# Performance work log

Measured on AMD Instinct MI355X. Metric: run time of the kernel, lower is better.

Reference implementation:

```python
import jax, jax.numpy as jnp
import numpy as np

S = 100        # sos_token_num
H = 12         # num heads
LY = 3         # number of residual blocks
NEG = -100.0   # attention-bias masking value


def layer_norm(x, w, b, eps=1e-5):
    u = jnp.mean(x, -1, keepdims=True)
    v = jnp.mean((x - u) ** 2, -1, keepdims=True)
    return (x - u) / jnp.sqrt(v + eps) * w + b


def quick_gelu(x):
    return x * jax.nn.sigmoid(1.702 * x)


def l2norm(x, eps=1e-12):
    return x / jnp.maximum(jnp.linalg.norm(x, axis=-1, keepdims=True), eps)


def setup_inputs() -> dict:
    key = jax.random.key(0)
    ks = iter(jax.random.split(key, 32))
    n, c, hh, ww, out_dim = 2, 768, 32, 32, 512
    r = lambda shape, s=1.0: jax.random.normal(next(ks), shape, jnp.float32) * s
    return dict(
        cls_token=r((1, n, c)),
        pix_feat=r((n, c, hh, ww)),
        last_surgery=r((1 + hh * ww, n, c)),
        attn_bias=r((n, 1, S, hh, ww)),
        qkv_w=r((LY, 3 * c, c), 0.02), qkv_b=jnp.zeros((LY, 3 * c)),
        proj_w=r((LY, c, c), 0.02), proj_b=jnp.zeros((LY, c)),
        ln1_w=jnp.ones((LY, c)), ln1_b=jnp.zeros((LY, c)),
        ln2_w=jnp.ones((LY, c)), ln2_b=jnp.zeros((LY, c)),
        fc_w=r((LY, 4 * c, c), 0.02), fc_b=jnp.zeros((LY, 4 * c)),
        fc2_w=r((LY, c, 4 * c), 0.02), fc2_b=jnp.zeros((LY, c)),
        lnp_w=jnp.ones((c,)), lnp_b=jnp.zeros((c,)),
        proj_out=r((c, out_dim), 0.02),
    )


def reference(cls_token, pix_feat, last_surgery, attn_bias,
              qkv_w, qkv_b, proj_w, proj_b,
              ln1_w, ln1_b, ln2_w, ln2_b,
              fc_w, fc_b, fc2_w, fc2_b,
              lnp_w, lnp_b, proj_out):
    n, c, hh, ww = pix_feat.shape
    L = hh * ww
    N = S + 1 + L
    d = c // H
    scale = d ** -0.5

    # ---- assemble token streams (batch-first [n, N, c]) ----
    pix_tok = pix_feat.reshape(n, c, L).transpose(2, 0, 1)          # [L, n, c]
    x = jnp.concatenate([jnp.broadcast_to(cls_token, (S, n, c)), cls_token, pix_tok], 0)
    x_sur = jnp.concatenate([jnp.broadcast_to(last_surgery[0:1], (S, n, c)), last_surgery], 0)
    xo = x.transpose(1, 0, 2)      # 'original' stream  [n, N, c]
    xs = x_sur.transpose(1, 0, 2)  # 'surgery'  stream  [n, N, c]

    # ---- build attention biases (identity downsample: bias already at (h, w)) ----
    base = jnp.zeros((N, N), jnp.float32)
    base = base.at[:, :S].set(NEG)
    base = base.at[jnp.arange(S), jnp.arange(S)].set(0.0)
    base = base.at[:S, S].set(NEG)
    plain = jnp.broadcast_to(base, (n, H, N, N))
    bias = jnp.broadcast_to(attn_bias, (n, H, S, hh, ww)).reshape(n, H, S, L)
    biased = plain.at[:, :, :S, S + 1:].set(bias)   # sos rows attend to pixels via bias

    def attention(t, l):
        # t: [n, N, c] (post-ln_1); returns (surgery_res, ori_res)
        qkv = (t @ qkv_w[l].T + qkv_b[l]).reshape(n, N, 3, H, d).transpose(2, 0, 3, 1, 4)
        q, k, v = qkv[0], qkv[1], qkv[2]   # each [n, H, N, d]
        def attend(q_, k_, mask):
            a = jax.nn.softmax(jnp.einsum('bhnd,bhmd->bhnm', q_, k_) * scale + mask, axis=-1)
            o = jnp.einsum('bhnm,bhmd->bhnd', a, v).transpose(0, 2, 1, 3).reshape(n, N, c)
            return o @ proj_w[l].T + proj_b[l]
        x_ori_res = attend(q, k, biased)   # standard pass, biased mask (attn_mask[0])
        x_res = attend(v, v, plain)        # q = k = v surgery pass (attn_mask[1])
        return x_res, x_ori_res

    for l in range(LY):
        t = layer_norm(xo, ln1_w[l], ln1_b[l])
        res_sur, res_ori = attention(t, l)
        xo = xo + res_ori
        xo = xo + (quick_gelu(layer_norm(xo, ln2_w[l], ln2_b[l]) @ fc_w[l].T + fc_b[l]) @ fc2_w[l].T + fc2_b[l])
        xs = xs + res_sur

    # ---- heads ----
    sos = l2norm(layer_norm(xo[:, :S], lnp_w, lnp_b) @ proj_out)          # [n, S, out]
    img = l2norm(layer_norm(xs[:, S:], lnp_w, lnp_b) @ proj_out)          # [n, 1+L, out]
    img = img[:, 1:, :].transpose(0, 2, 1).reshape(n, proj_out.shape[1], hh, ww)
    return sos, img
```

## Files before the change

### kernel.cpp

```cpp
#include <hip/hip_runtime.h>
#include <math.h>


constexpr int Cc = 768;
constexpr int Ss = 100;
constexpr int Hh = 12;
constexpr int Ll = 1024;
constexpr int Nn = 1125;
constexpr int NB = 2;
constexpr float QS = 0.18033688011112042f;
constexpr float LOG2E = 1.4426950408889634f;

typedef unsigned short u16;
typedef __attribute__((ext_vector_type(8))) short short8v;
typedef __attribute__((ext_vector_type(8))) unsigned short ushort8v;
typedef __attribute__((ext_vector_type(4))) float f32x4;
typedef __attribute__((ext_vector_type(4))) unsigned int u32x4;

__device__ inline u16 f2bf(float f) {
  unsigned u = __builtin_bit_cast(unsigned int, f);
  unsigned r = u + 0x7fffu + ((u >> 16) & 1u);
  return (u16)(r >> 16);
}
__device__ inline float bf2f(u16 v) {
  return __builtin_bit_cast(float, (unsigned int)v << 16);
}
__device__ inline unsigned cvtpk(float lo, float hi) {
  unsigned r;
  asm("v_cvt_pk_bf16_f32 %0, %1, %2" : "=v"(r) : "v"(lo), "v"(hi));
  return r;
}

__device__ inline int swz(int row, int col) {
  return (row << 6) + ((((col >> 3) ^ (row & 7)) << 3) | (col & 7));
}

__global__ __launch_bounds__(256) void assemble_kernel(
    const float* __restrict__ cls, const float* __restrict__ pix,
    const float* __restrict__ sur, float* __restrict__ xo, float* __restrict__ xs) {
  int idx = blockIdx.x * 256 + (int)threadIdx.x;
  int total = NB * Nn * Cc;
  if (idx >= total) return;
  int ch = idx % Cc;
  int t  = (idx / Cc) % Nn;
  int b  = idx / (Cc * Nn);
  float vo, vs;
  if (t <= Ss) vo = cls[b * Cc + ch];
  else         vo = pix[(size_t)b * Cc * Ll + (size_t)ch * Ll + (t - Ss - 1)];
  if (t < Ss)  vs = sur[b * Cc + ch];
  else         vs = sur[(size_t)(t - Ss) * NB * Cc + b * Cc + ch];
  xo[idx] = vo;
  xs[idx] = vs;
}

constexpr int CN0 = 3 * 2304 * 768;
constexpr int CN1 = 3 * 768 * 768;
constexpr int CN2 = 3 * 3072 * 768;
constexpr int CN3 = 3 * 768 * 3072;
__global__ __launch_bounds__(256) void cvt4_kernel(
    const float* __restrict__ s0, const float* __restrict__ s1,
    const float* __restrict__ s2, const float* __restrict__ s3,
    u16* __restrict__ dst) {
  int i4 = (blockIdx.x * 256 + (int)threadIdx.x) * 4;
  if (i4 >= CN0 + CN1 + CN2 + CN3) return;
  const float* src; int off;
  if (i4 < CN0)             { src = s0; off = i4; }
  else if (i4 < CN0 + CN1)  { src = s1; off = i4 - CN0; }
  else if (i4 < CN0 + CN1 + CN2) { src = s2; off = i4 - CN0 - CN1; }
  else                      { src = s3; off = i4 - CN0 - CN1 - CN2; }
  float4 v = *(const float4*)(src + off);
  *(ushort4*)(dst + i4) = make_ushort4(f2bf(v.x), f2bf(v.y), f2bf(v.z), f2bf(v.w));
}

__global__ __launch_bounds__(256) void transpose_po_kernel(
    const float* __restrict__ in, u16* __restrict__ out) {
  int id = blockIdx.x * 256 + (int)threadIdx.x;
  if (id >= 512 * 768) return;
  int nidx = id / 768, k = id - nidx * 768;
  out[id] = f2bf(in[(size_t)k * 512 + nidx]);
}

__global__ __launch_bounds__(256) void ln_kernel(
    const float* __restrict__ X, const float* __restrict__ w, const float* __restrict__ b,
    u16* __restrict__ Y, int rows_per_b, int row_off) {
  int r = blockIdx.x;
  int bb = r / rows_per_b;
  int i  = r % rows_per_b;
  const float* x = X + ((size_t)bb * Nn + row_off + i) * Cc;
  u16* y = Y + (size_t)r * Cc;
  int tid = (int)threadIdx.x;
  float v0 = x[tid], v1 = x[tid + 256], v2 = x[tid + 512];
  float s = v0 + v1 + v2;
  __shared__ float sbuf[4];
  for (int off = 32; off; off >>= 1) s += __shfl_xor(s, off);
  if ((tid & 63) == 0) sbuf[tid >> 6] = s;
  __syncthreads();
  float mean = (sbuf[0] + sbuf[1] + sbuf[2] + sbuf[3]) * (1.0f / Cc);
  float d0 = v0 - mean, d1 = v1 - mean, d2 = v2 - mean;
  float q = d0 * d0 + d1 * d1 + d2 * d2;
  __syncthreads();
  for (int off = 32; off; off >>= 1) q += __shfl_xor(q, off);
  if ((tid & 63) == 0) sbuf[tid >> 6] = q;
  __syncthreads();
  float var = (sbuf[0] + sbuf[1] + sbuf[2] + sbuf[3]) * (1.0f / Cc);
  float inv = rsqrtf(var + 1e-5f);
  y[tid]       = f2bf(d0 * inv * w[tid]       + b[tid]);
  y[tid + 256] = f2bf(d1 * inv * w[tid + 256] + b[tid + 256]);
  y[tid + 512] = f2bf(d2 * inv * w[tid + 512] + b[tid + 512]);
}

__global__ __launch_bounds__(256) void gemm64_kernel(
    const u16* __restrict__ A0, const u16* __restrict__ A1,
    const u16* __restrict__ B, const float* __restrict__ bias,
    const float* __restrict__ res0, const float* __restrict__ res1,
    float* __restrict__ outf0, float* __restrict__ outf1,
    u16* __restrict__ outb0, u16* __restrict__ outb1,
    int M, int N, int K, int act) {
  __shared__ __align__(16) u16 Als[64 * 64];
  __shared__ __align__(16) u16 Bls[128 * 64];
  int zz = blockIdx.z;
  const u16* A = zz ? A1 : A0;
  const float* res = zz ? res1 : res0;
  float* outf = zz ? outf1 : outf0;
  u16* outb = zz ? outb1 : outb0;
  int tid = (int)threadIdx.x;
  int wave = tid >> 6, lane = tid & 63, g = lane >> 4, li = lane & 15;
  int row0 = blockIdx.y * 64, col0 = blockIdx.x * 128;

  const u16* aptr[2]; int dA[2];
#pragma unroll
  for (int j = 0; j < 2; ++j) {
    int ca = tid + j * 256;
    int r = ca >> 3, c8 = ca & 7;
    dA[j] = (r << 6) + ((c8 ^ (r & 7)) << 3);
    int ra = row0 + r; if (ra > M - 1) ra = M - 1;
    aptr[j] = A + (size_t)ra * K + (c8 << 3);
  }
  const u16* bptr[4]; int dB[4];
#pragma unroll
  for (int j = 0; j < 4; ++j) {
    int cb = tid + j * 256;
    int r = cb >> 3, c8 = cb & 7;
    dB[j] = (r << 6) + ((c8 ^ (r & 7)) << 3);
    bptr[j] = B + (size_t)(col0 + r) * K + (c8 << 3);
  }

  f32x4 acc[4][2];
#pragma unroll
  for (int mi = 0; mi < 4; ++mi)
#pragma unroll
    for (int ni = 0; ni < 2; ++ni) acc[mi][ni] = (f32x4){0.f, 0.f, 0.f, 0.f};

  for (int k0 = 0; k0 < K; k0 += 64) {
    ushort8v ta[2], tb[4];
#pragma unroll
    for (int j = 0; j < 2; ++j) ta[j] = *(const ushort8v*)(aptr[j] + k0);
#pragma unroll
    for (int j = 0; j < 4; ++j) tb[j] = *(const ushort8v*)(bptr[j] + k0);
    __syncthreads();
#pragma unroll
    for (int j = 0; j < 2; ++j) *(ushort8v*)&Als[dA[j]] = ta[j];
#pragma unroll
    for (int j = 0; j < 4; ++j) *(ushort8v*)&Bls[dB[j]] = tb[j];
    __syncthreads();
#pragma unroll
    for (int kc = 0; kc < 2; ++kc) {
      short8v af[4], bfr[2];
#pragma unroll
      for (int mi = 0; mi < 4; ++mi) {
        int rr = mi * 16 + li;
        af[mi] = *(const short8v*)&Als[(rr << 6) + (((kc * 4 + g) ^ (rr & 7)) << 3)];
      }
#pragma unroll
      for (int ni = 0; ni < 2; ++ni) {
        int rb = wave * 32 + ni * 16 + li;
        bfr[ni] = *(const short8v*)&Bls[(rb << 6) + (((kc * 4 + g) ^ (rb & 7)) << 3)];
      }
#pragma unroll
      for (int mi = 0; mi < 4; ++mi)
#pragma unroll
        for (int ni = 0; ni < 2; ++ni)
          acc[mi][ni] = __builtin_amdgcn_mfma_f32_16x16x32_bf16(af[mi], bfr[ni], acc[mi][ni], 0, 0, 0);
    }
  }

#pragma unroll
  for (int mi = 0; mi < 4; ++mi) {
#pragma unroll
    for (int r = 0; r < 4; ++r) {
      int m = row0 + mi * 16 + g * 4 + r;
      if (m >= M) continue;
#pragma unroll
      for (int ni = 0; ni < 2; ++ni) {
        int n = col0 + wave * 32 + ni * 16 + li;
        float v = acc[mi][ni][r];
        if (bias) v += bias[n];
        if (act)  v = v / (1.0f + __expf(-1.702f * v));
        if (res)  v += res[(size_t)m * N + n];
        if (outf) outf[(size_t)m * N + n] = v;
        else      outb[(size_t)m * N + n] = f2bf(v);
      }
    }
  }
}

__global__ __launch_bounds__(256) void attn_kernel(
    const u16* __restrict__ qkv, const float* __restrict__ abias,
    u16* __restrict__ ao, u16* __restrict__ as_) {
  __shared__ __align__(16) u16 Klds[64 * 64];
  __shared__ __align__(16) u16 Vt[64 * 64];
  int id = (int)blockIdx.x;
  int virt = (id & 7) * 114 + (id >> 3);
  int gid = virt / 19;
  int qt  = virt - gid * 19;
  int z   = gid / 24;
  int bh  = gid - z * 24;
  int b = bh / Hh, h = bh - b * Hh;
  int tid = (int)threadIdx.x;
  int wave = tid >> 6, lane = tid & 63, g = lane >> 4, li = lane & 15;
  bool sosq = qt >= 17;
  u16* outp = z ? as_ : ao;

  int qbase = sosq ? (qt - 17) * 64 + wave * 16 : Ss + qt * 64 + wave * 16;
  int qtok = qbase + li;
  int qcap = sosq ? 99 : 1124;
  if (qtok > qcap) qtok = qcap;
  int qoff = z ? 2 * Cc + h * 64 : h * 64;
  int koff = z ? 2 * Cc + h * 64 : Cc + h * 64;
  int voff = 2 * Cc + h * 64;

  short8v qf[2];
  {
    const u16* qp = qkv + ((size_t)b * Nn + qtok) * 2304 + qoff;
#pragma unroll
    for (int kc = 0; kc < 2; ++kc) {
      ushort8v a = *(const ushort8v*)(qp + kc * 32 + g * 8);
      u32x4 w;
#pragma unroll
      for (int jj = 0; jj < 4; ++jj)
        w[jj] = cvtpk(bf2f(a[2 * jj]) * QS, bf2f(a[2 * jj + 1]) * QS);
      qf[kc] = __builtin_bit_cast(short8v, w);
    }
  }

  int skey = tid >> 2;
  int sd0  = (tid & 3) << 4;
  int rot  = tid & 3;
  int prow = 16 * (2 * (skey >> 5) + ((skey >> 2) & 1)) + 4 * ((skey >> 3) & 3) + (skey & 3);
  int kI0 = swz(prow, sd0), kI1 = swz(prow, sd0 + 8);

  const int KOFF[4] = {0, 4, 32, 36};

  f32x4 oacc[4];
#pragma unroll
  for (int dt = 0; dt < 4; ++dt) oacc[dt] = (f32x4){0.f, 0.f, 0.f, 0.f};
  float mrow = -1e30f, lrow = 0.f;

  for (int kt = 0; kt < 17; ++kt) {
    int ktok0 = sosq ? (kt == 0 ? (qt - 17) * 64 : Ss + 1 + (kt - 1) * 64)
                     : Ss + kt * 64;
    __syncthreads();
    {
      int ktok = ktok0 + skey;
      if (ktok <= 1124) {
        const u16* kp = qkv + ((size_t)b * Nn + ktok) * 2304;
        *(ushort8v*)&Klds[kI0] = *(const ushort8v*)(kp + koff + sd0);
        *(ushort8v*)&Klds[kI1] = *(const ushort8v*)(kp + koff + sd0 + 8);
        ushort8v v0 = *(const ushort8v*)(kp + voff + sd0);
        ushort8v v1 = *(const ushort8v*)(kp + voff + sd0 + 8);
        u16 vv[16];
#pragma unroll
        for (int j = 0; j < 8; ++j) { vv[j] = v0[j]; vv[j + 8] = v1[j]; }
#pragma unroll
        for (int mm = 0; mm < 16; ++mm) {
          int jj = (mm + rot) & 15;
          Vt[swz(sd0 + jj, skey)] = vv[jj];
        }
      } else {
        ushort8v zv = (ushort8v)0;
        *(ushort8v*)&Klds[kI0] = zv;
        *(ushort8v*)&Klds[kI1] = zv;
#pragma unroll
        for (int mm = 0; mm < 16; ++mm) Vt[swz(sd0 + mm, skey)] = 0;
      }
    }
    __syncthreads();

    f32x4 sacc[4];
#pragma unroll
    for (int nt = 0; nt < 4; ++nt) sacc[nt] = (f32x4){0.f, 0.f, 0.f, 0.f};
    __builtin_amdgcn_s_setprio(1);
#pragma unroll
    for (int kc = 0; kc < 2; ++kc) {
#pragma unroll
      for (int nt = 0; nt < 4; ++nt) {
        short8v kb = *(const short8v*)&Klds[swz(nt * 16 + li, kc * 32 + g * 8)];
        sacc[nt] = __builtin_amdgcn_mfma_f32_16x16x32_bf16(kb, qf[kc], sacc[nt], 0, 0, 0);
      }
    }
    __builtin_amdgcn_s_setprio(0);

    if (sosq) {
      if (kt == 0) {
        int qloc = wave * 16 + li;
#pragma unroll
        for (int nt = 0; nt < 4; ++nt)
#pragma unroll
          for (int r = 0; r < 4; ++r)
            if (KOFF[nt] + 8 * g + r != qloc) sacc[nt][r] = -1e30f;
      } else if (z == 0) {
        const float* bp = abias + ((size_t)b * Ss + qtok) * Ll + (ktok0 - 101) + 8 * g;
#pragma unroll
        for (int nt = 0; nt < 4; ++nt) {
          float4 bv = *(const float4*)(bp + KOFF[nt]);
          sacc[nt][0] = fmaf(bv.x, LOG2E, sacc[nt][0]);
          sacc[nt][1] = fmaf(bv.y, LOG2E, sacc[nt][1]);
          sacc[nt][2] = fmaf(bv.z, LOG2E, sacc[nt][2]);
          sacc[nt][3] = fmaf(bv.w, LOG2E, sacc[nt][3]);
        }
      }
    } else if (kt == 16) {
#pragma unroll
      for (int nt = 0; nt < 4; ++nt)
#pragma unroll
        for (int r = 0; r < 4; ++r)
          if (ktok0 + KOFF[nt] + 8 * g + r > 1124) sacc[nt][r] = -1e30f;
    }

    float rmax = -1e30f;
#pragma unroll
    for (int nt = 0; nt < 4; ++nt)
#pragma unroll
      for (int r = 0; r < 4; ++r) rmax = fmaxf(rmax, sacc[nt][r]);
    rmax = fmaxf(rmax, __shfl_xor(rmax, 16));
    rmax = fmaxf(rmax, __shfl_xor(rmax, 32));
    float mnew = fmaxf(mrow, rmax);
    float fac = __builtin_amdgcn_exp2f(mrow - mnew);
    mrow = mnew;
    float psum = 0.f;
#pragma unroll
    for (int nt = 0; nt < 4; ++nt)
#pragma unroll
      for (int r = 0; r < 4; ++r) {
        float e = __builtin_amdgcn_exp2f(sacc[nt][r] - mnew);
        sacc[nt][r] = e;
        psum += e;
      }
    psum += __shfl_xor(psum, 16);
    psum += __shfl_xor(psum, 32);
    lrow = lrow * fac + psum;
#pragma unroll
    for (int dt = 0; dt < 4; ++dt) oacc[dt] *= fac;

    __builtin_amdgcn_s_setprio(1);
#pragma unroll
    for (int kcp = 0; kcp < 2; ++kcp) {
      u32x4 pwv;
#pragma unroll
      for (int w = 0; w < 4; ++w) {
        int nt = 2 * kcp + (w >> 1);
        int r0 = (w & 1) * 2;
        pwv[w] = cvtpk(sacc[nt][r0], sacc[nt][r0 + 1]);
      }
      short8v pb = __builtin_bit_cast(short8v, pwv);
#pragma unroll
      for (int dt = 0; dt < 4; ++dt) {
        short8v va = *(const short8v*)&Vt[swz(dt * 16 + li, kcp * 32 + g * 8)];
        oacc[dt] = __builtin_amdgcn_mfma_f32_16x16x32_bf16(va, pb, oacc[dt], 0, 0, 0);
      }
    }
    __builtin_amdgcn_s_setprio(0);
  }

  int tok = qbase + li;
  if (tok <= qcap) {
    float inv = 1.0f / lrow;
    u16* op = outp + ((size_t)b * Nn + tok) * Cc + h * 64 + g * 4;
#pragma unroll
    for (int dt = 0; dt < 4; ++dt) {
      unsigned lo = cvtpk(oacc[dt][0] * inv, oacc[dt][1] * inv);
      unsigned hi = cvtpk(oacc[dt][2] * inv, oacc[dt][3] * inv);
      uint2 o2; o2.x = lo; o2.y = hi;
      *(uint2*)(op + dt * 16) = o2;
    }
  }
}

__global__ __launch_bounds__(256) void l2norm_sos_kernel(
    const float* __restrict__ Xp, float* __restrict__ out) {
  int r = blockIdx.x;
  int tid = (int)threadIdx.x;
  const float* x = Xp + (size_t)r * 512;
  float v0 = x[tid], v1 = x[tid + 256];
  float s = v0 * v0 + v1 * v1;
  __shared__ float sbuf[4];
  for (int off = 32; off; off >>= 1) s += __shfl_xor(s, off);
  if ((tid & 63) == 0) sbuf[tid >> 6] = s;
  __syncthreads();
  float tot = sbuf[0] + sbuf[1] + sbuf[2] + sbuf[3];
  float inv = 1.0f / fmaxf(sqrtf(tot), 1e-12f);
  out[(size_t)r * 512 + tid]       = v0 * inv;
  out[(size_t)r * 512 + tid + 256] = v1 * inv;
}

__global__ __launch_bounds__(256) void l2norm_img_kernel(
    const float* __restrict__ Xp, float* __restrict__ out) {
  int r = blockIdx.x;
  int b = r / 1025, ti = r % 1025;
  int tid = (int)threadIdx.x;
  const float* x = Xp + (size_t)r * 512;
  float v0 = x[tid], v1 = x[tid + 256];
  float s = v0 * v0 + v1 * v1;
  __shared__ float sbuf[4];
  for (int off = 32; off; off >>= 1) s += __shfl_xor(s, off);
  if ((tid & 63) == 0) sbuf[tid >> 6] = s;
  __syncthreads();
  float tot = sbuf[0] + sbuf[1] + sbuf[2] + sbuf[3];
  if (ti == 0) return;
  float inv = 1.0f / fmaxf(sqrtf(tot), 1e-12f);
  float* o = out + (size_t)b * 512 * 1024 + (ti - 1);
  o[(size_t)tid * 1024]         = v0 * inv;
  o[(size_t)(tid + 256) * 1024] = v1 * inv;
}

extern "C" void kernel_launch(void* const* d_in, const int* in_sizes, int n_in,
                              void* d_out, int out_size, void* d_ws, size_t ws_size,
                              hipStream_t stream) {
  const float* cls      = (const float*)d_in[0];
  const float* pix      = (const float*)d_in[1];
  const float* sur      = (const float*)d_in[2];
  const float* abias    = (const float*)d_in[3];
  const float* qkv_w    = (const float*)d_in[4];
  const float* qkv_b    = (const float*)d_in[5];
  const float* proj_w   = (const float*)d_in[6];
  const float* proj_b   = (const float*)d_in[7];
  const float* ln1_w    = (const float*)d_in[8];
  const float* ln1_b    = (const float*)d_in[9];
  const float* ln2_w    = (const float*)d_in[10];
  const float* ln2_b    = (const float*)d_in[11];
  const float* fc_w     = (const float*)d_in[12];
  const float* fc_b     = (const float*)d_in[13];
  const float* fc2_w    = (const float*)d_in[14];
  const float* fc2_b    = (const float*)d_in[15];
  const float* lnp_w    = (const float*)d_in[16];
  const float* lnp_b    = (const float*)d_in[17];
  const float* proj_o   = (const float*)d_in[18];
  float* out = (float*)d_out;

  const size_t SZ = (size_t)NB * Nn * Cc;
  float* xo      = (float*)d_ws;
  float* xs      = xo + SZ;
  float* head_pj = xs + SZ;
  u16* tln_bf = (u16*)(head_pj + 2250 * 512);
  u16* act_bf = tln_bf + (size_t)2250 * 768;
  u16* ao_bf  = act_bf + (size_t)2250 * 3072;
  u16* as_bf  = ao_bf + (size_t)2250 * 768;
  u16* wq_bf  = as_bf + (size_t)2250 * 768;
  u16* wp_bf  = wq_bf + (size_t)CN0;
  u16* wf_bf  = wp_bf + (size_t)CN1;
  u16* w2_bf  = wf_bf + (size_t)CN2;
  u16* wo_bf  = w2_bf + (size_t)CN3;

  assemble_kernel<<<6750, 256, 0, stream>>>(cls, pix, sur, xo, xs);
  cvt4_kernel<<<20736, 256, 0, stream>>>(qkv_w, proj_w, fc_w, fc2_w, wq_bf);
  transpose_po_kernel<<<1536, 256, 0, stream>>>(proj_o, wo_bf);

  for (int l = 0; l < 3; ++l) {
    ln_kernel<<<2250, 256, 0, stream>>>(xo, ln1_w + l * 768, ln1_b + l * 768, tln_bf, Nn, 0);
    gemm64_kernel<<<dim3(18, 36, 1), 256, 0, stream>>>(
        tln_bf, tln_bf, wq_bf + (size_t)l * 2304 * 768, qkv_b + l * 2304,
        nullptr, nullptr, nullptr, nullptr, act_bf, act_bf, 2250, 2304, 768, 0);
    attn_kernel<<<912, 256, 0, stream>>>(act_bf, abias, ao_bf, as_bf);
    gemm64_kernel<<<dim3(6, 36, 2), 256, 0, stream>>>(
        ao_bf, as_bf, wp_bf + (size_t)l * 768 * 768, proj_b + l * 768,
        xo, xs, xo, xs, nullptr, nullptr, 2250, 768, 768, 0);
    ln_kernel<<<2250, 256, 0, stream>>>(xo, ln2_w + l * 768, ln2_b + l * 768, tln_bf, Nn, 0);
    gemm64_kernel<<<dim3(24, 36, 1), 256, 0, stream>>>(
        tln_bf, tln_bf, wf_bf + (size_t)l * 3072 * 768, fc_b + l * 3072,
        nullptr, nullptr, nullptr, nullptr, act_bf, act_bf, 2250, 3072, 768, 1);
    gemm64_kernel<<<dim3(6, 36, 1), 256, 0, stream>>>(
        act_bf, act_bf, w2_bf + (size_t)l * 768 * 3072, fc2_b + l * 768,
        xo, xo, xo, xo, nullptr, nullptr, 2250, 768, 3072, 0);
  }

  ln_kernel<<<200, 256, 0, stream>>>(xo, lnp_w, lnp_b, tln_bf, 100, 0);
  ln_kernel<<<2050, 256, 0, stream>>>(xs, lnp_w, lnp_b, tln_bf + 200 * 768, 1025, 100);
  gemm64_kernel<<<dim3(4, 36, 1), 256, 0, stream>>>(
      tln_bf, tln_bf, wo_bf, nullptr,
      nullptr, nullptr, head_pj, head_pj, nullptr, nullptr, 2250, 512, 768, 0);
  l2norm_sos_kernel<<<200, 256, 0, stream>>>(head_pj, out);
  l2norm_img_kernel<<<2050, 256, 0, stream>>>(head_pj + 200 * 512, out + 102400);
}
```

Before: 851.9 us.

## Pre-transpose V for attention and use direct global-to-LDS loads in GEMM

Adds a kernel that writes V per batch and head in transposed [d, token] layout, so attention can load V tiles with vector loads instead of scattered per-element LDS transposes. Key tiles are realigned and out-of-range keys are masked per element, with the bias read as scalar gathers. The GEMM now streams A and B tiles into LDS with global_load_lds, drops the XOR swizzle, and raises wave priority around the MFMA block. Costs are an extra kernel launch and V round-trip through memory, possible LDS bank conflicts from the unswizzled layout, and more scalar bias loads; a v_max3 reduction is also added.

```diff
diff --git a/kernel.cpp b/kernel.cpp
--- a/kernel.cpp
+++ b/kernel.cpp
@@ -8,10 +8,12 @@
 constexpr int Ll = 1024;
 constexpr int Nn = 1125;
 constexpr int NB = 2;
+constexpr int VTS = 1216;
 constexpr float QS = 0.18033688011112042f;
 constexpr float LOG2E = 1.4426950408889634f;
 
 typedef unsigned short u16;
+typedef unsigned int u32;
 typedef __attribute__((ext_vector_type(8))) short short8v;
 typedef __attribute__((ext_vector_type(8))) unsigned short ushort8v;
 typedef __attribute__((ext_vector_type(4))) float f32x4;
@@ -29,6 +31,16 @@
   unsigned r;
   asm("v_cvt_pk_bf16_f32 %0, %1, %2" : "=v"(r) : "v"(lo), "v"(hi));
   return r;
+}
+__device__ inline float max3f(float a, float b, float c) {
+  float r;
+  asm("v_max3_f32 %0, %1, %2, %3" : "=v"(r) : "v"(a), "v"(b), "v"(c));
+  return r;
+}
+__device__ __forceinline__ void gl_lds16(const u16* g, u16* l) {
+  __builtin_amdgcn_global_load_lds(
+      (const __attribute__((address_space(1))) u32*)g,
+      (__attribute__((address_space(3))) u32*)l, 16, 0, 0);
 }
 
 __device__ inline int swz(int row, int col) {
@@ -78,6 +90,36 @@
   if (id >= 512 * 768) return;
   int nidx = id / 768, k = id - nidx * 768;
   out[id] = f2bf(in[(size_t)k * 512 + nidx]);
+}
+
+__global__ __launch_bounds__(256) void vtrans_kernel(
+    const u16* __restrict__ qkv, u16* __restrict__ vtg) {
+  __shared__ u16 tile[64][72];
+  int tt = blockIdx.x;
+  int bh = blockIdx.y;
+  int b = bh / Hh, h = bh - b * Hh;
+  int tid = (int)threadIdx.x;
+  {
+    int tl = tid >> 2, c0 = (tid & 3) << 4;
+    int tok = tt * 64 + tl;
+    int tokc = tok > 1124 ? 1124 : tok;
+    const u16* src = qkv + ((size_t)(b * Nn + tokc)) * 2304 + 2 * Cc + h * 64 + c0;
+    ushort8v v0 = *(const ushort8v*)src;
+    ushort8v v1 = *(const ushort8v*)(src + 8);
+    if (tok > 1124) { v0 = (ushort8v)0; v1 = (ushort8v)0; }
+    *(ushort8v*)&tile[tl][c0] = v0;
+    *(ushort8v*)&tile[tl][c0 + 8] = v1;
+  }
+  __syncthreads();
+  {
+    int d = tid >> 2, t0 = (tid & 3) << 4;
+    ushort8v o0, o1;
+#pragma unroll
+    for (int j = 0; j < 8; ++j) { o0[j] = tile[t0 + j][d]; o1[j] = tile[t0 + 8 + j][d]; }
+    size_t orow = ((size_t)bh * 64 + d) * VTS + tt * 64 + t0;
+    *(ushort8v*)&vtg[orow] = o0;
+    *(ushort8v*)&vtg[orow + 8] = o1;
+  }
 }
 
 __global__ __launch_bounds__(256) void ln_kernel(
@@ -127,22 +169,19 @@
   int wave = tid >> 6, lane = tid & 63, g = lane >> 4, li = lane & 15;
   int row0 = blockIdx.y * 64, col0 = blockIdx.x * 128;
 
-  const u16* aptr[2]; int dA[2];
-#pragma unroll
-  for (int j = 0; j < 2; ++j) {
-    int ca = tid + j * 256;
-    int r = ca >> 3, c8 = ca & 7;
-    dA[j] = (r << 6) + ((c8 ^ (r & 7)) << 3);
-    int ra = row0 + r; if (ra > M - 1) ra = M - 1;
-    aptr[j] = A + (size_t)ra * K + (c8 << 3);
-  }
-  const u16* bptr[4]; int dB[4];
+  int lr = lane >> 3, lc = (lane & 7) << 3;
+  int ar0 = row0 + wave * 16 + lr;      if (ar0 > M - 1) ar0 = M - 1;
+  int ar1 = row0 + wave * 16 + 8 + lr;  if (ar1 > M - 1) ar1 = M - 1;
+  const u16* as0 = A + (size_t)ar0 * K + lc;
+  const u16* as1 = A + (size_t)ar1 * K + lc;
+  u16* al0 = &Als[wave * 1024];
+  u16* al1 = &Als[wave * 1024 + 512];
+  const u16* bs[4]; u16* bl[4];
 #pragma unroll
   for (int j = 0; j < 4; ++j) {
-    int cb = tid + j * 256;
-    int r = cb >> 3, c8 = cb & 7;
-    dB[j] = (r << 6) + ((c8 ^ (r & 7)) << 3);
-    bptr[j] = B + (size_t)(col0 + r) * K + (c8 << 3);
+    int brow = wave * 32 + j * 8 + lr;
+    bs[j] = B + (size_t)(col0 + brow) * K + lc;
+    bl[j] = &Bls[(wave * 4 + j) * 512];
   }
 
   f32x4 acc[4][2];
@@ -152,35 +191,28 @@
     for (int ni = 0; ni < 2; ++ni) acc[mi][ni] = (f32x4){0.f, 0.f, 0.f, 0.f};
 
   for (int k0 = 0; k0 < K; k0 += 64) {
-    ushort8v ta[2], tb[4];
-#pragma unroll
-    for (int j = 0; j < 2; ++j) ta[j] = *(const ushort8v*)(aptr[j] + k0);
-#pragma unroll
-    for (int j = 0; j < 4; ++j) tb[j] = *(const ushort8v*)(bptr[j] + k0);
-    __syncthreads();
-#pragma unroll
-    for (int j = 0; j < 2; ++j) *(ushort8v*)&Als[dA[j]] = ta[j];
-#pragma unroll
-    for (int j = 0; j < 4; ++j) *(ushort8v*)&Bls[dB[j]] = tb[j];
+    if (k0) __syncthreads();
+    gl_lds16(as0 + k0, al0);
+    gl_lds16(as1 + k0, al1);
+#pragma unroll
+    for (int j = 0; j < 4; ++j) gl_lds16(bs[j] + k0, bl[j]);
     __syncthreads();
 #pragma unroll
     for (int kc = 0; kc < 2; ++kc) {
       short8v af[4], bfr[2];
 #pragma unroll
-      for (int mi = 0; mi < 4; ++mi) {
-        int rr = mi * 16 + li;
-        af[mi] = *(const short8v*)&Als[(rr << 6) + (((kc * 4 + g) ^ (rr & 7)) << 3)];
-      }
-#pragma unroll
-      for (int ni = 0; ni < 2; ++ni) {
-        int rb = wave * 32 + ni * 16 + li;
-        bfr[ni] = *(const short8v*)&Bls[(rb << 6) + (((kc * 4 + g) ^ (rb & 7)) << 3)];
-      }
+      for (int mi = 0; mi < 4; ++mi)
+        af[mi] = *(const short8v*)&Als[(mi * 16 + li) * 64 + kc * 32 + g * 8];
+#pragma unroll
+      for (int ni = 0; ni < 2; ++ni)
+        bfr[ni] = *(const short8v*)&Bls[(wave * 32 + ni * 16 + li) * 64 + kc * 32 + g * 8];
+      __builtin_amdgcn_s_setprio(1);
 #pragma unroll
       for (int mi = 0; mi < 4; ++mi)
 #pragma unroll
         for (int ni = 0; ni < 2; ++ni)
           acc[mi][ni] = __builtin_amdgcn_mfma_f32_16x16x32_bf16(af[mi], bfr[ni], acc[mi][ni], 0, 0, 0);
+      __builtin_amdgcn_s_setprio(0);
     }
   }
 
@@ -205,7 +237,8 @@
 }
 
 __global__ __launch_bounds__(256) void attn_kernel(
-    const u16* __restrict__ qkv, const float* __restrict__ abias,
+    const u16* __restrict__ qkv, const u16* __restrict__ vtg,
+    const float* __restrict__ abias,
     u16* __restrict__ ao, u16* __restrict__ as_) {
   __shared__ __align__(16) u16 Klds[64 * 64];
   __shared__ __align__(16) u16 Vt[64 * 64];
@@ -227,7 +260,6 @@
   if (qtok > qcap) qtok = qcap;
   int qoff = z ? 2 * Cc + h * 64 : h * 64;
   int koff = z ? 2 * Cc + h * 64 : Cc + h * 64;
-  int voff = 2 * Cc + h * 64;
 
   short8v qf[2];
   {
@@ -245,9 +277,11 @@
 
   int skey = tid >> 2;
   int sd0  = (tid & 3) << 4;
-  int rot  = tid & 3;
   int prow = 16 * (2 * (skey >> 5) + ((skey >> 2) & 1)) + 4 * ((skey >> 3) & 3) + (skey & 3);
-  int kI0 = swz(prow, sd0), kI1 = swz(prow, sd0 + 8);
+  int kK0 = swz(prow, sd0), kK1 = swz(prow, sd0 + 8);
+  int vI0 = swz(skey, sd0), vI1 = swz(skey, sd0 + 8);
+  const u16* kbase = qkv + (size_t)b * Nn * 2304 + koff + sd0;
+  const u16* vbase = vtg + ((size_t)bh * 64 + skey) * VTS + sd0;
 
   const int KOFF[4] = {0, 4, 32, 36};
 
@@ -256,33 +290,22 @@
   for (int dt = 0; dt < 4; ++dt) oacc[dt] = (f32x4){0.f, 0.f, 0.f, 0.f};
   float mrow = -1e30f, lrow = 0.f;
 
-  for (int kt = 0; kt < 17; ++kt) {
-    int ktok0 = sosq ? (kt == 0 ? (qt - 17) * 64 : Ss + 1 + (kt - 1) * 64)
-                     : Ss + kt * 64;
+  int NT = sosq ? 18 : 17;
+  for (int kt = 0; kt < NT; ++kt) {
+    int t0 = sosq ? (kt == 0 ? (qt - 17) * 64 : 64 * kt + 32) : 96 + 64 * kt;
     __syncthreads();
     {
-      int ktok = ktok0 + skey;
-      if (ktok <= 1124) {
-        const u16* kp = qkv + ((size_t)b * Nn + ktok) * 2304;
-        *(ushort8v*)&Klds[kI0] = *(const ushort8v*)(kp + koff + sd0);
-        *(ushort8v*)&Klds[kI1] = *(const ushort8v*)(kp + koff + sd0 + 8);
-        ushort8v v0 = *(const ushort8v*)(kp + voff + sd0);
-        ushort8v v1 = *(const ushort8v*)(kp + voff + sd0 + 8);
-        u16 vv[16];
-#pragma unroll
-        for (int j = 0; j < 8; ++j) { vv[j] = v0[j]; vv[j + 8] = v1[j]; }
-#pragma unroll
-        for (int mm = 0; mm < 16; ++mm) {
-          int jj = (mm + rot) & 15;
-          Vt[swz(sd0 + jj, skey)] = vv[jj];
-        }
-      } else {
-        ushort8v zv = (ushort8v)0;
-        *(ushort8v*)&Klds[kI0] = zv;
-        *(ushort8v*)&Klds[kI1] = zv;
-#pragma unroll
-        for (int mm = 0; mm < 16; ++mm) Vt[swz(sd0 + mm, skey)] = 0;
-      }
+      int ktok = t0 + skey; if (ktok > 1124) ktok = 1124;
+      const u16* kp = kbase + (size_t)ktok * 2304;
+      ushort8v k0v = *(const ushort8v*)kp;
+      ushort8v k1v = *(const ushort8v*)(kp + 8);
+      const u16* vp = vbase + t0;
+      ushort8v v0 = *(const ushort8v*)vp;
+      ushort8v v1 = *(const ushort8v*)(vp + 8);
+      *(ushort8v*)&Klds[kK0] = k0v;
+      *(ushort8v*)&Klds[kK1] = k1v;
+      *(ushort8v*)&Vt[vI0] = v0;
+      *(ushort8v*)&Vt[vI1] = v1;
     }
     __syncthreads();
 
@@ -300,38 +323,59 @@
     }
     __builtin_amdgcn_s_setprio(0);
 
-    if (sosq) {
+    int tg = t0 + 8 * g;
+    if (!sosq) {
       if (kt == 0) {
-        int qloc = wave * 16 + li;
 #pragma unroll
         for (int nt = 0; nt < 4; ++nt)
 #pragma unroll
           for (int r = 0; r < 4; ++r)
-            if (KOFF[nt] + 8 * g + r != qloc) sacc[nt][r] = -1e30f;
+            if (tg + KOFF[nt] + r < 100) sacc[nt][r] = -1e30f;
+      } else if (kt == 16) {
+#pragma unroll
+        for (int nt = 0; nt < 4; ++nt)
+#pragma unroll
+          for (int r = 0; r < 4; ++r)
+            if (tg + KOFF[nt] + r > 1124) sacc[nt][r] = -1e30f;
+      }
+    } else {
+      if (kt == 0) {
+#pragma unroll
+        for (int nt = 0; nt < 4; ++nt)
+#pragma unroll
+          for (int r = 0; r < 4; ++r)
+            if (tg + KOFF[nt] + r != qtok) sacc[nt][r] = -1e30f;
       } else if (z == 0) {
-        const float* bp = abias + ((size_t)b * Ss + qtok) * Ll + (ktok0 - 101) + 8 * g;
-#pragma unroll
-        for (int nt = 0; nt < 4; ++nt) {
-          float4 bv = *(const float4*)(bp + KOFF[nt]);
-          sacc[nt][0] = fmaf(bv.x, LOG2E, sacc[nt][0]);
-          sacc[nt][1] = fmaf(bv.y, LOG2E, sacc[nt][1]);
-          sacc[nt][2] = fmaf(bv.z, LOG2E, sacc[nt][2]);
-          sacc[nt][3] = fmaf(bv.w, LOG2E, sacc[nt][3]);
-        }
-      }
-    } else if (kt == 16) {
-#pragma unroll
-      for (int nt = 0; nt < 4; ++nt)
-#pragma unroll
-        for (int r = 0; r < 4; ++r)
-          if (ktok0 + KOFF[nt] + 8 * g + r > 1124) sacc[nt][r] = -1e30f;
-    }
-
-    float rmax = -1e30f;
-#pragma unroll
-    for (int nt = 0; nt < 4; ++nt)
-#pragma unroll
-      for (int r = 0; r < 4; ++r) rmax = fmaxf(rmax, sacc[nt][r]);
+        const float* bp = abias + ((size_t)b * Ss + qtok) * Ll;
+#pragma unroll
+        for (int nt = 0; nt < 4; ++nt)
+#pragma unroll
+          for (int r = 0; r < 4; ++r) {
+            int tok = tg + KOFF[nt] + r;
+            int bi = tok - 101; bi = bi < 0 ? 0 : bi; bi = bi > 1023 ? 1023 : bi;
+            float bv = bp[bi];
+            bool bad = (tok < 101) | (tok > 1124);
+            sacc[nt][r] = bad ? -1e30f : fmaf(bv, LOG2E, sacc[nt][r]);
+          }
+      } else {
+#pragma unroll
+        for (int nt = 0; nt < 4; ++nt)
+#pragma unroll
+          for (int r = 0; r < 4; ++r) {
+            int tok = tg + KOFF[nt] + r;
+            if ((tok < 101) | (tok > 1124)) sacc[nt][r] = -1e30f;
+          }
+      }
+    }
+
+    float rmax = max3f(sacc[0][0], sacc[0][1], sacc[0][2]);
+    rmax = max3f(rmax, sacc[0][3], sacc[1][0]);
+    rmax = max3f(rmax, sacc[1][1], sacc[1][2]);
+    rmax = max3f(rmax, sacc[1][3], sacc[2][0]);
+    rmax = max3f(rmax, sacc[2][1], sacc[2][2]);
+    rmax = max3f(rmax, sacc[2][3], sacc[3][0]);
+    rmax = max3f(rmax, sacc[3][1], sacc[3][2]);
+    rmax = fmaxf(rmax, sacc[3][3]);
     rmax = fmaxf(rmax, __shfl_xor(rmax, 16));
     rmax = fmaxf(rmax, __shfl_xor(rmax, 32));
     float mnew = fmaxf(mrow, rmax);
@@ -460,6 +504,7 @@
   u16* wf_bf  = wp_bf + (size_t)CN1;
   u16* w2_bf  = wf_bf + (size_t)CN2;
   u16* wo_bf  = w2_bf + (size_t)CN3;
+  u16* vtg    = wo_bf + (size_t)512 * 768;
 
   assemble_kernel<<<6750, 256, 0, stream>>>(cls, pix, sur, xo, xs);
   cvt4_kernel<<<20736, 256, 0, stream>>>(qkv_w, proj_w, fc_w, fc2_w, wq_bf);
@@ -470,7 +515,8 @@
     gemm64_kernel<<<dim3(18, 36, 1), 256, 0, stream>>>(
         tln_bf, tln_bf, wq_bf + (size_t)l * 2304 * 768, qkv_b + l * 2304,
         nullptr, nullptr, nullptr, nullptr, act_bf, act_bf, 2250, 2304, 768, 0);
-    attn_kernel<<<912, 256, 0, stream>>>(act_bf, abias, ao_bf, as_bf);
+    vtrans_kernel<<<dim3(19, 24), 256, 0, stream>>>(act_bf, vtg);
+    attn_kernel<<<912, 256, 0, stream>>>(act_bf, vtg, abias, ao_bf, as_bf);
     gemm64_kernel<<<dim3(6, 36, 2), 256, 0, stream>>>(
         ao_bf, as_bf, wp_bf + (size_t)l * 768 * 768, proj_b + l * 768,
         xo, xs, xo, xs, nullptr, nullptr, 2250, 768, 768, 0);
```

After: 800.9 us. 6.0% less time.
